# Kernel optimization log

Measured on AMD Instinct MI355X. Metric: run time of the kernel, lower is better.

## Reference

```python
import jax, jax.numpy as jnp
import numpy as np

WORLD_SIZE = 8
M = 4096
N = 4096
K_LOCAL = 1024  # full K = WORLD_SIZE * K_LOCAL = 8192


def setup_inputs() -> dict:
    key = jax.random.key(0)
    k1, k2 = jax.random.split(key)
    # Per-rank activation shard [R, M, K_local] and weight shard [R, N, K_local]
    inp = jax.random.normal(k1, (WORLD_SIZE, M, K_LOCAL), dtype=jnp.float32) * 0.02
    w = jax.random.normal(k2, (WORLD_SIZE, N, K_LOCAL), dtype=jnp.float32) * 0.02
    return {"input": inp, "weight": w}


def reference(input, weight):
    # Each rank r computes a partial GEMM: input[r] @ weight[r].T -> [M, N].
    # Reduce(-scatter) sums partials over ranks; the single einsum contracts
    # both the rank axis (the all-reduce part) and K_local (the GEMM part).
    full = jnp.einsum("rmk,rnk->mn", input, weight)  # [M, N]
    R = input.shape[0]
    # Scatter: rank r receives rows [r*M/R : (r+1)*M/R] -> stacked [R, M/R, N]
    return full.reshape(R, full.shape[0] // R, full.shape[1])
```

## Files before the change

### kernel.cpp

```cpp
#include <hip/hip_runtime.h>
#include <cstdint>
#include <cstddef>


#define M_DIM 4096
#define N_DIM 4096
#define K_DIM 8192
#define K_LOCAL 1024
#define RANKS 8

typedef __bf16 bf16x8 __attribute__((ext_vector_type(8)));
typedef float f32x4 __attribute__((ext_vector_type(4)));

__device__ __forceinline__ unsigned short f2bf(float f) {
    unsigned int u = __float_as_uint(f);
    unsigned int r = (u + 0x7fffu + ((u >> 16) & 1u)) >> 16;
    return (unsigned short)r;
}

__global__ __launch_bounds__(256) void convert_cast(
    const float* __restrict__ srcA, unsigned short* __restrict__ dstA,
    const float* __restrict__ srcB, unsigned short* __restrict__ dstB,
    int blocks_per_tensor) {
    const float* src = srcA;
    unsigned short* dst = dstA;
    int b = blockIdx.x;
    if (b >= blocks_per_tensor) { b -= blocks_per_tensor; src = srcB; dst = dstB; }
    size_t base = (size_t)b * 4096 + threadIdx.x * 4;
#pragma unroll
    for (int i = 0; i < 4; ++i) {
        size_t e = base + i * 1024;
        f32x4 v = __builtin_nontemporal_load((const f32x4*)(src + e));
        ushort4 o;
        o.x = f2bf(v.x); o.y = f2bf(v.y); o.z = f2bf(v.z); o.w = f2bf(v.w);
        *(ushort4*)(dst + e) = o;
    }
}

__device__ __forceinline__ void gll16(const unsigned short* g, unsigned short* l) {
    __builtin_amdgcn_global_load_lds(
        (const __attribute__((address_space(1))) void*)g,
        (__attribute__((address_space(3))) void*)l,
        16, 0, 0);
}

__device__ __forceinline__ int k_off(int t) {
    return ((t >> 4) << 22) | ((t & 15) << 6);
}

#define VM8 asm volatile("s_waitcnt vmcnt(8)" ::: "memory")
#define VM0 asm volatile("s_waitcnt vmcnt(0)" ::: "memory")
#define VMNONE ((void)0)
#define BAR __builtin_amdgcn_s_barrier();

#define STAGE_A(TOFF, HALF, PBUF) { \
    _Pragma("unroll") for (int j_ = 0; j_ < 2; ++j_) \
        gll16(A + (size_t)((TOFF) + (HALF) * 131072 + thrA[j_]), \
              smem + (PBUF) * 16384 + (HALF) * 8192 + ldsOff[j_]); }

#define STAGE_B(TOFF, HALF, PBUF) { \
    _Pragma("unroll") for (int j_ = 0; j_ < 2; ++j_) \
        gll16(B + (size_t)((TOFF) + (HALF) * 131072 + thrB[j_]), \
              smem + 32768 + (PBUF) * 16384 + (HALF) * 8192 + ldsOff[j_]); }

#define READ_A(DST, BASE, MOFF) { \
    _Pragma("unroll") for (int ks_ = 0; ks_ < 2; ++ks_) \
        _Pragma("unroll") for (int mm_ = 0; mm_ < 4; ++mm_) \
            DST[ks_][mm_] = *(const bf16x8*)&(BASE)[(((MOFF) + mm_) * 16 + l15) * 64 + (ks_ ? swz1 : swz0)]; }

#define READ_B(DST, BASE, NJ0) { \
    _Pragma("unroll") for (int ks_ = 0; ks_ < 2; ++ks_) \
        _Pragma("unroll") for (int nn_ = 0; nn_ < 2; ++nn_) \
            DST[ks_][nn_] = *(const bf16x8*)&(BASE)[(bRowBase + ((NJ0) + nn_) * 16 + l15) * 64 + (ks_ ? swz1 : swz0)]; }

#define QUAD(AF, BF, MI0, NJ0) { \
    __builtin_amdgcn_s_setprio(1); \
    _Pragma("unroll") for (int ks_ = 0; ks_ < 2; ++ks_) \
        _Pragma("unroll") for (int mm_ = 0; mm_ < 4; ++mm_) \
            _Pragma("unroll") for (int nn_ = 0; nn_ < 2; ++nn_) \
                acc[(MI0) + mm_][(NJ0) + nn_] = __builtin_amdgcn_mfma_f32_16x16x32_bf16( \
                    AF[ks_][mm_], BF[ks_][nn_], acc[(MI0) + mm_][(NJ0) + nn_], 0, 0, 0); \
    __builtin_amdgcn_s_setprio(0); }

#define KTILE(PBUF, KT, S, SR, VMOP) { \
    const int t2off_ = k_off((KT) + 2); \
    unsigned short* aC_ = smem + (PBUF) * 16384 + wmIdx * 8192; \
    unsigned short* bC_ = smem + 32768 + (PBUF) * 16384 + bHalfSel * 8192; \
    unsigned short* aN_ = smem + ((PBUF) ^ 1) * 16384 + wmIdx * 8192; \
    unsigned short* bN_ = smem + 32768 + ((PBUF) ^ 1) * 16384 + bHalfSel * 8192; \
     \
    READ_A(aHi, aC_, 4) \
    QUAD(aLo, bLo, 0, 0) \
    BAR \
     \
    READ_B(bHi, bC_, 2) \
    QUAD(aHi, bLo, 4, 0) \
    VMOP; \
    BAR \
     \
    if (S) { STAGE_A(t2off_, 0, (PBUF)) } \
    QUAD(aLo, bHi, 0, 2) \
    if (SR) { READ_A(aLo, aN_, 0) } \
    BAR \
     \
    if (SR) { READ_B(bLo, bN_, 0) } \
    if (S) { STAGE_A(t2off_, 1, (PBUF)) STAGE_B(t2off_, 0, (PBUF)) STAGE_B(t2off_, 1, (PBUF)) } \
    QUAD(aHi, bHi, 4, 2) \
    BAR \
}

__global__ __launch_bounds__(512, 2) void gemm_bf16_8ph(
    const unsigned short* __restrict__ A,
    const unsigned short* __restrict__ B,
    float* __restrict__ C) {
    extern __shared__ unsigned short smem[];

    const int tid = threadIdx.x;
    const int lane = tid & 63;
    const int wave = tid >> 6;
    const int wmIdx = wave >> 2;
    const int wn = wave & 3;
    const int l15 = lane & 15;
    const int l4 = lane >> 4;
    const int bHalfSel = wn >> 1;
    const int bRowBase = (wn & 1) * 64;

    const int bid = blockIdx.x;
    const int xcd = bid & 7;
    const int idx = bid >> 3;
    const int tm = (xcd >> 2) * 8 + (idx >> 2);
    const int tn = (xcd & 3) * 4 + (idx & 3);
    const int bm0 = tm * 256;
    const int bn0 = tn * 256;

    int thrA[2], thrB[2], ldsOff[2];
#pragma unroll
    for (int j = 0; j < 2; ++j) {
        int cc = j * 512 + tid;
        int row = cc >> 3;
        int col = ((cc & 7) ^ (row & 7)) * 8;
        thrA[j] = (bm0 + row) * K_LOCAL + col;
        thrB[j] = (bn0 + row) * K_LOCAL + col;
        ldsOff[j] = cc * 8;
    }

    const int swz0 = ((0 + l4) ^ (l15 & 7)) * 8;
    const int swz1 = ((4 + l4) ^ (l15 & 7)) * 8;

    bf16x8 aLo[2][4], aHi[2][4], bLo[2][2], bHi[2][2];
    f32x4 acc[8][4] = {};

    STAGE_A(0, 0, 0)
    STAGE_A(0, 1, 0)
    STAGE_B(0, 0, 0)
    STAGE_B(0, 1, 0)
    STAGE_A(64, 0, 1)
    STAGE_A(64, 1, 1)
    STAGE_B(64, 0, 1)
    STAGE_B(64, 1, 1)
    VM8;
    BAR
    {
        unsigned short* a0_ = smem + wmIdx * 8192;
        unsigned short* b0_ = smem + 32768 + bHalfSel * 8192;
        READ_A(aLo, a0_, 0)
        READ_B(bLo, b0_, 0)
    }

#pragma unroll 1
    for (int kt = 0; kt < 126; kt += 2) {
        KTILE(0, kt, 1, 1, VM0)
        KTILE(1, kt + 1, 1, 1, VM0)
    }
    KTILE(0, 126, 0, 1, VM0)
    KTILE(1, 127, 0, 0, VMNONE)

#pragma unroll
    for (int mi = 0; mi < 8; ++mi) {
        int row0 = bm0 + wmIdx * 128 + mi * 16 + l4 * 4;
#pragma unroll
        for (int nj = 0; nj < 4; ++nj) {
            int col = bn0 + wn * 64 + nj * 16 + l15;
#pragma unroll
            for (int r = 0; r < 4; ++r)
                C[(size_t)(row0 + r) * N_DIM + col] = acc[mi][nj][r];
        }
    }
}

__global__ __launch_bounds__(256) void gemm_bf16_128(
    const unsigned short* __restrict__ A,
    const unsigned short* __restrict__ B,
    float* __restrict__ C) {
    __shared__ __align__(16) unsigned short As[128 * 64];
    __shared__ __align__(16) unsigned short Bs[128 * 64];

    const int tid = threadIdx.x;
    const int lane = tid & 63;
    const int wave = tid >> 6;
    const int wm = (wave >> 1) * 64;
    const int wnn = (wave & 1) * 64;
    const int l15 = lane & 15;
    const int l4 = lane >> 4;

    const int bid = blockIdx.x;
    const int xcd = bid & 7;
    const int q = bid >> 3;
    const int st = (q >> 2) * 8 + xcd;
    const int pos = q & 3;
    const int bm0 = ((st >> 4) * 2 + (pos >> 1)) * 128;
    const int bn0 = ((st & 15) * 2 + (pos & 1)) * 128;

    const unsigned short* ga[4];
    const unsigned short* gb[4];
    int lo[4];
#pragma unroll
    for (int p = 0; p < 4; ++p) {
        int cc = p * 256 + tid;
        int row = cc >> 3;
        int cpos = cc & 7;
        int col = (cpos ^ (row & 7)) * 8;
        ga[p] = A + (size_t)(bm0 + row) * K_LOCAL + col;
        gb[p] = B + (size_t)(bn0 + row) * K_LOCAL + col;
        lo[p] = cc * 8;
    }

    const int swz0 = ((l4 + 0) ^ (l15 & 7)) * 8;
    const int swz1 = ((l4 + 4) ^ (l15 & 7)) * 8;
    const int a_row = (wm + l15) * 64;
    const int b_row = (wnn + l15) * 64;

    f32x4 acc[4][4] = {};

    for (int r = 0; r < RANKS; ++r) {
        const size_t roff = (size_t)r * (M_DIM * (size_t)K_LOCAL);
        for (int kl = 0; kl < K_LOCAL; kl += 64) {
#pragma unroll
            for (int p = 0; p < 4; ++p) {
                gll16(ga[p] + roff + kl, &As[lo[p]]);
                gll16(gb[p] + roff + kl, &Bs[lo[p]]);
            }
            __syncthreads();
#pragma unroll
            for (int ks = 0; ks < 2; ++ks) {
                const int swz = ks ? swz1 : swz0;
                bf16x8 af[4], bfr[4];
#pragma unroll
                for (int i = 0; i < 4; ++i)
                    af[i] = *(const bf16x8*)&As[a_row + i * 16 * 64 + swz];
#pragma unroll
                for (int j = 0; j < 4; ++j)
                    bfr[j] = *(const bf16x8*)&Bs[b_row + j * 16 * 64 + swz];
#pragma unroll
                for (int i = 0; i < 4; ++i)
#pragma unroll
                    for (int j = 0; j < 4; ++j)
                        acc[i][j] = __builtin_amdgcn_mfma_f32_16x16x32_bf16(
                            af[i], bfr[j], acc[i][j], 0, 0, 0);
            }
            __syncthreads();
        }
    }

#pragma unroll
    for (int i = 0; i < 4; ++i) {
        int row0 = bm0 + wm + i * 16 + l4 * 4;
#pragma unroll
        for (int j = 0; j < 4; ++j) {
            int col = bn0 + wnn + j * 16 + l15;
#pragma unroll
            for (int r = 0; r < 4; ++r)
                C[(size_t)(row0 + r) * N_DIM + col] = acc[i][j][r];
        }
    }
}

__global__ void gemm_naive(const float* __restrict__ A, const float* __restrict__ B,
                           float* __restrict__ C) {
    __shared__ float As[16][17];
    __shared__ float Bs[16][17];
    int tx = threadIdx.x, ty = threadIdx.y;
    int m = blockIdx.y * 16 + ty;
    int n0 = blockIdx.x * 16;
    float accv = 0.f;
    for (int kt = 0; kt < K_DIM; kt += 16) {
        int r = kt >> 10;
        int k = (kt & 1023) + tx;
        As[ty][tx] = A[((size_t)r * M_DIM + m) * K_LOCAL + k];
        Bs[ty][tx] = B[((size_t)r * N_DIM + (n0 + ty)) * K_LOCAL + k];
        __syncthreads();
#pragma unroll
        for (int kk = 0; kk < 16; ++kk) accv += As[ty][kk] * Bs[tx][kk];
        __syncthreads();
    }
    C[(size_t)m * N_DIM + n0 + tx] = accv;
}

extern "C" void kernel_launch(void* const* d_in, const int* in_sizes, int n_in,
                              void* d_out, int out_size, void* d_ws, size_t ws_size,
                              hipStream_t stream) {
    const float* inp = (const float*)d_in[0];
    const float* wgt = (const float*)d_in[1];
    float* out = (float*)d_out;

    const size_t elems = (size_t)M_DIM * K_DIM;
    const size_t need = 2 * elems * sizeof(unsigned short);

    if (ws_size >= need) {
        unsigned short* Abf = (unsigned short*)d_ws;
        unsigned short* Bbf = Abf + elems;
        const int bpt = (int)(elems / 4096);
        convert_cast<<<bpt * 2, 256, 0, stream>>>(inp, Abf, wgt, Bbf, bpt);

        static int dynOK = -1;
        if (dynOK < 0) {
            dynOK = (hipFuncSetAttribute((const void*)gemm_bf16_8ph,
                                         hipFuncAttributeMaxDynamicSharedMemorySize,
                                         131072) == hipSuccess)
                        ? 1
                        : 0;
        }
        if (dynOK) {
            gemm_bf16_8ph<<<256, 512, 131072, stream>>>(Abf, Bbf, out);
        } else {
            gemm_bf16_128<<<1024, 256, 0, stream>>>(Abf, Bbf, out);
        }
    } else {
        dim3 grid(N_DIM / 16, M_DIM / 16);
        dim3 block(16, 16);
        gemm_naive<<<grid, block, 0, stream>>>(inp, wgt, out);
    }
}
```

Measured before the change: 266.1 us.

## Switch GEMM to 128x256 tiles with 256 threads and single-buffered A

Replaces the 256x256, 512-thread GEMM kernel with a 128x256 tile kernel using 4 waves and 512 blocks. A is now single-buffered in LDS and reloaded each k-tile, while B stays double-buffered and is staged in two halves. The prefetch distance drops from two k-tiles to one, and waits become partial vmcnt(4). LDS per block shrinks so two blocks fit per CU, but reuse per tile falls and the pipeline is shallower, which may expose more global-load latency.

```diff
diff --git a/kernel.cpp b/kernel.cpp
--- a/kernel.cpp
+++ b/kernel.cpp
@@ -48,30 +48,34 @@
     return ((t >> 4) << 22) | ((t & 15) << 6);
 }
 
-#define VM8 asm volatile("s_waitcnt vmcnt(8)" ::: "memory")
+#define VM4 asm volatile("s_waitcnt vmcnt(4)" ::: "memory")
 #define VM0 asm volatile("s_waitcnt vmcnt(0)" ::: "memory")
 #define VMNONE ((void)0)
 #define BAR __builtin_amdgcn_s_barrier();
 
-#define STAGE_A(TOFF, HALF, PBUF) { \
-    _Pragma("unroll") for (int j_ = 0; j_ < 2; ++j_) \
-        gll16(A + (size_t)((TOFF) + (HALF) * 131072 + thrA[j_]), \
-              smem + (PBUF) * 16384 + (HALF) * 8192 + ldsOff[j_]); }
-
-#define STAGE_B(TOFF, HALF, PBUF) { \
-    _Pragma("unroll") for (int j_ = 0; j_ < 2; ++j_) \
-        gll16(B + (size_t)((TOFF) + (HALF) * 131072 + thrB[j_]), \
-              smem + 32768 + (PBUF) * 16384 + (HALF) * 8192 + ldsOff[j_]); }
-
-#define READ_A(DST, BASE, MOFF) { \
+#define STAGE_A(TOFF) { \
+    _Pragma("unroll") for (int j_ = 0; j_ < 4; ++j_) \
+        gll16(A + (size_t)((TOFF) + thrA[j_]), smem + ldsA[j_]); }
+
+#define STAGE_BS1(TOFF, PBUF) { \
+    _Pragma("unroll") for (int j_ = 0; j_ < 4; ++j_) \
+        gll16(B + (size_t)((TOFF) + thrB[j_]), \
+              smem + 8192 + (PBUF) * 16384 + ldsB[j_]); }
+
+#define STAGE_BS2(TOFF, PBUF) { \
+    _Pragma("unroll") for (int j_ = 0; j_ < 4; ++j_) \
+        gll16(B + (size_t)((TOFF) + 32 * K_LOCAL + thrB[j_]), \
+              smem + 8192 + (PBUF) * 16384 + 2048 + ldsB[j_]); }
+
+#define READ_A(DST, MOFF) { \
     _Pragma("unroll") for (int ks_ = 0; ks_ < 2; ++ks_) \
         _Pragma("unroll") for (int mm_ = 0; mm_ < 4; ++mm_) \
-            DST[ks_][mm_] = *(const bf16x8*)&(BASE)[(((MOFF) + mm_) * 16 + l15) * 64 + (ks_ ? swz1 : swz0)]; }
-
-#define READ_B(DST, BASE, NJ0) { \
+            DST[ks_][mm_] = *(const bf16x8*)&smem[(((MOFF) + mm_) * 16 + l15) * 64 + (ks_ ? swz1 : swz0)]; }
+
+#define READ_B(DST, NJ0, PBUF) { \
     _Pragma("unroll") for (int ks_ = 0; ks_ < 2; ++ks_) \
         _Pragma("unroll") for (int nn_ = 0; nn_ < 2; ++nn_) \
-            DST[ks_][nn_] = *(const bf16x8*)&(BASE)[(bRowBase + ((NJ0) + nn_) * 16 + l15) * 64 + (ks_ ? swz1 : swz0)]; }
+            DST[ks_][nn_] = *(const bf16x8*)&smem[8192 + (PBUF) * 16384 + wn * 4096 + (((NJ0) + nn_) * 16 + l15) * 64 + (ks_ ? swz1 : swz0)]; }
 
 #define QUAD(AF, BF, MI0, NJ0) { \
     __builtin_amdgcn_s_setprio(1); \
@@ -82,34 +86,30 @@
                     AF[ks_][mm_], BF[ks_][nn_], acc[(MI0) + mm_][(NJ0) + nn_], 0, 0, 0); \
     __builtin_amdgcn_s_setprio(0); }
 
-#define KTILE(PBUF, KT, S, SR, VMOP) { \
-    const int t2off_ = k_off((KT) + 2); \
-    unsigned short* aC_ = smem + (PBUF) * 16384 + wmIdx * 8192; \
-    unsigned short* bC_ = smem + 32768 + (PBUF) * 16384 + bHalfSel * 8192; \
-    unsigned short* aN_ = smem + ((PBUF) ^ 1) * 16384 + wmIdx * 8192; \
-    unsigned short* bN_ = smem + 32768 + ((PBUF) ^ 1) * 16384 + bHalfSel * 8192; \
+#define KTILE(PBUF, KT, S, SR, VMP1, VMP3) { \
+    const int t1off_ = k_off((KT) + 1); \
      \
-    READ_A(aHi, aC_, 4) \
+    READ_A(aHi, 4) \
+    if (S) { STAGE_BS1(t1off_, (PBUF) ^ 1) } \
     QUAD(aLo, bLo, 0, 0) \
+    VMP1; \
     BAR \
      \
-    READ_B(bHi, bC_, 2) \
+    READ_B(bHi, 2, PBUF) \
     QUAD(aHi, bLo, 4, 0) \
-    VMOP; \
     BAR \
      \
-    if (S) { STAGE_A(t2off_, 0, (PBUF)) } \
+    if (S) { STAGE_A(t1off_) STAGE_BS2(t1off_, (PBUF) ^ 1) } \
     QUAD(aLo, bHi, 0, 2) \
-    if (SR) { READ_A(aLo, aN_, 0) } \
+    VMP3; \
     BAR \
      \
-    if (SR) { READ_B(bLo, bN_, 0) } \
-    if (S) { STAGE_A(t2off_, 1, (PBUF)) STAGE_B(t2off_, 0, (PBUF)) STAGE_B(t2off_, 1, (PBUF)) } \
+    if (SR) { READ_A(aLo, 0) READ_B(bLo, 0, (PBUF) ^ 1) } \
     QUAD(aHi, bHi, 4, 2) \
     BAR \
 }
 
-__global__ __launch_bounds__(512, 2) void gemm_bf16_8ph(
+__global__ __launch_bounds__(256, 2) void gemm_bf16_2blk(
     const unsigned short* __restrict__ A,
     const unsigned short* __restrict__ B,
     float* __restrict__ C) {
@@ -117,31 +117,29 @@
 
     const int tid = threadIdx.x;
     const int lane = tid & 63;
-    const int wave = tid >> 6;
-    const int wmIdx = wave >> 2;
-    const int wn = wave & 3;
+    const int wn = tid >> 6;
     const int l15 = lane & 15;
     const int l4 = lane >> 4;
-    const int bHalfSel = wn >> 1;
-    const int bRowBase = (wn & 1) * 64;
 
     const int bid = blockIdx.x;
     const int xcd = bid & 7;
     const int idx = bid >> 3;
-    const int tm = (xcd >> 2) * 8 + (idx >> 2);
-    const int tn = (xcd & 3) * 4 + (idx & 3);
-    const int bm0 = tm * 256;
+    const int tm = (xcd >> 1) * 8 + (idx >> 3);
+    const int tn = (xcd & 1) * 8 + (idx & 7);
+    const int bm0 = tm * 128;
     const int bn0 = tn * 256;
 
-    int thrA[2], thrB[2], ldsOff[2];
-#pragma unroll
-    for (int j = 0; j < 2; ++j) {
-        int cc = j * 512 + tid;
-        int row = cc >> 3;
-        int col = ((cc & 7) ^ (row & 7)) * 8;
-        thrA[j] = (bm0 + row) * K_LOCAL + col;
-        thrB[j] = (bn0 + row) * K_LOCAL + col;
-        ldsOff[j] = cc * 8;
+    int thrA[4], ldsA[4], thrB[4], ldsB[4];
+#pragma unroll
+    for (int j = 0; j < 4; ++j) {
+        int cc = j * 256 + tid;
+        int rowA = cc >> 3;
+        thrA[j] = (bm0 + rowA) * K_LOCAL + (((cc & 7) ^ (rowA & 7)) * 8);
+        ldsA[j] = cc * 8;
+        int blk = cc >> 8;
+        int rr = (cc & 255) >> 3;
+        thrB[j] = (bn0 + blk * 64 + rr) * K_LOCAL + (((cc & 7) ^ (rr & 7)) * 8);
+        ldsB[j] = blk * 4096 + (cc & 255) * 8;
     }
 
     const int swz0 = ((0 + l4) ^ (l15 & 7)) * 8;
@@ -150,34 +148,25 @@
     bf16x8 aLo[2][4], aHi[2][4], bLo[2][2], bHi[2][2];
     f32x4 acc[8][4] = {};
 
-    STAGE_A(0, 0, 0)
-    STAGE_A(0, 1, 0)
-    STAGE_B(0, 0, 0)
-    STAGE_B(0, 1, 0)
-    STAGE_A(64, 0, 1)
-    STAGE_A(64, 1, 1)
-    STAGE_B(64, 0, 1)
-    STAGE_B(64, 1, 1)
-    VM8;
+    STAGE_A(0)
+    STAGE_BS1(0, 0)
+    STAGE_BS2(0, 0)
+    VM0;
     BAR
-    {
-        unsigned short* a0_ = smem + wmIdx * 8192;
-        unsigned short* b0_ = smem + 32768 + bHalfSel * 8192;
-        READ_A(aLo, a0_, 0)
-        READ_B(bLo, b0_, 0)
-    }
+    READ_A(aLo, 0)
+    READ_B(bLo, 0, 0)
 
 #pragma unroll 1
     for (int kt = 0; kt < 126; kt += 2) {
-        KTILE(0, kt, 1, 1, VM0)
-        KTILE(1, kt + 1, 1, 1, VM0)
-    }
-    KTILE(0, 126, 0, 1, VM0)
-    KTILE(1, 127, 0, 0, VMNONE)
+        KTILE(0, kt, 1, 1, VM4, VM4)
+        KTILE(1, kt + 1, 1, 1, VM4, VM4)
+    }
+    KTILE(0, 126, 1, 1, VM4, VM4)
+    KTILE(1, 127, 0, 0, VM0, VMNONE)
 
 #pragma unroll
     for (int mi = 0; mi < 8; ++mi) {
-        int row0 = bm0 + wmIdx * 128 + mi * 16 + l4 * 4;
+        int row0 = bm0 + mi * 16 + l4 * 4;
 #pragma unroll
         for (int nj = 0; nj < 4; ++nj) {
             int col = bn0 + wn * 64 + nj * 16 + l15;
@@ -314,14 +303,14 @@
 
         static int dynOK = -1;
         if (dynOK < 0) {
-            dynOK = (hipFuncSetAttribute((const void*)gemm_bf16_8ph,
+            dynOK = (hipFuncSetAttribute((const void*)gemm_bf16_2blk,
                                          hipFuncAttributeMaxDynamicSharedMemorySize,
-                                         131072) == hipSuccess)
+                                         81920) == hipSuccess)
                         ? 1
                         : 0;
         }
         if (dynOK) {
-            gemm_bf16_8ph<<<256, 512, 131072, stream>>>(Abf, Bbf, out);
+            gemm_bf16_2blk<<<512, 256, 81920, stream>>>(Abf, Bbf, out);
         } else {
             gemm_bf16_128<<<1024, 256, 0, stream>>>(Abf, Bbf, out);
         }
```

Result: slower. 284.8 us (+7.0%).

## Restructure GEMM k-loop to prefetch one tile ahead with a single barrier

Applied to the files above, without the earlier changes.

Changes the software pipeline from prefetching two K-tiles ahead, spread across four barrier-separated phases, to prefetching only the next tile into the other LDS buffer at the start of each K-tile. There is now one barrier per tile, plus a sched_barrier, instead of four. The intent is to cut synchronization overhead and let more MFMAs run between waits. The cost is less latency hiding: each tile now fully waits (vmcnt(0)) for loads issued in that same tile, which can stall on global memory latency.

```diff
diff --git a/kernel.cpp b/kernel.cpp
--- a/kernel.cpp
+++ b/kernel.cpp
@@ -48,7 +48,6 @@
     return ((t >> 4) << 22) | ((t & 15) << 6);
 }
 
-#define VM8 asm volatile("s_waitcnt vmcnt(8)" ::: "memory")
 #define VM0 asm volatile("s_waitcnt vmcnt(0)" ::: "memory")
 #define VMNONE ((void)0)
 #define BAR __builtin_amdgcn_s_barrier();
@@ -83,30 +82,25 @@
     __builtin_amdgcn_s_setprio(0); }
 
 #define KTILE(PBUF, KT, S, SR, VMOP) { \
-    const int t2off_ = k_off((KT) + 2); \
+    const int t1off_ = k_off((KT) + 1); \
     unsigned short* aC_ = smem + (PBUF) * 16384 + wmIdx * 8192; \
     unsigned short* bC_ = smem + 32768 + (PBUF) * 16384 + bHalfSel * 8192; \
     unsigned short* aN_ = smem + ((PBUF) ^ 1) * 16384 + wmIdx * 8192; \
     unsigned short* bN_ = smem + 32768 + ((PBUF) ^ 1) * 16384 + bHalfSel * 8192; \
      \
     READ_A(aHi, aC_, 4) \
+    if (S) { STAGE_A(t1off_, 0, (PBUF) ^ 1) STAGE_A(t1off_, 1, (PBUF) ^ 1) \
+             STAGE_B(t1off_, 0, (PBUF) ^ 1) STAGE_B(t1off_, 1, (PBUF) ^ 1) } \
     QUAD(aLo, bLo, 0, 0) \
-    BAR \
-     \
     READ_B(bHi, bC_, 2) \
     QUAD(aHi, bLo, 4, 0) \
+    QUAD(aLo, bHi, 0, 2) \
     VMOP; \
     BAR \
+    __builtin_amdgcn_sched_barrier(0); \
      \
-    if (S) { STAGE_A(t2off_, 0, (PBUF)) } \
-    QUAD(aLo, bHi, 0, 2) \
-    if (SR) { READ_A(aLo, aN_, 0) } \
-    BAR \
-     \
-    if (SR) { READ_B(bLo, bN_, 0) } \
-    if (S) { STAGE_A(t2off_, 1, (PBUF)) STAGE_B(t2off_, 0, (PBUF)) STAGE_B(t2off_, 1, (PBUF)) } \
+    if (SR) { READ_A(aLo, aN_, 0) READ_B(bLo, bN_, 0) } \
     QUAD(aHi, bHi, 4, 2) \
-    BAR \
 }
 
 __global__ __launch_bounds__(512, 2) void gemm_bf16_8ph(
@@ -154,25 +148,17 @@
     STAGE_A(0, 1, 0)
     STAGE_B(0, 0, 0)
     STAGE_B(0, 1, 0)
-    STAGE_A(64, 0, 1)
-    STAGE_A(64, 1, 1)
-    STAGE_B(64, 0, 1)
-    STAGE_B(64, 1, 1)
-    VM8;
+    VM0;
     BAR
-    {
-        unsigned short* a0_ = smem + wmIdx * 8192;
-        unsigned short* b0_ = smem + 32768 + bHalfSel * 8192;
-        READ_A(aLo, a0_, 0)
-        READ_B(bLo, b0_, 0)
-    }
+    READ_A(aLo, smem + wmIdx * 8192, 0)
+    READ_B(bLo, smem + 32768 + bHalfSel * 8192, 0)
 
 #pragma unroll 1
     for (int kt = 0; kt < 126; kt += 2) {
         KTILE(0, kt, 1, 1, VM0)
         KTILE(1, kt + 1, 1, 1, VM0)
     }
-    KTILE(0, 126, 0, 1, VM0)
+    KTILE(0, 126, 1, 1, VM0)
     KTILE(1, 127, 0, 0, VMNONE)
 
 #pragma unroll
```

New measurement: 259.3 us (median of 3 runs). -2.6%, faster.
